# Kernel optimization log

Hardware: AMD Instinct MI355X
Metric: run time of the kernel (lower is better)

## Reference

```python
import jax, jax.numpy as jnp
import numpy as np

K = 3          # per-row / per-col topk, from init kwarg k
THRESHOLD = 0.0


def setup_inputs() -> dict:
    key = jax.random.key(0)
    k1, k2 = jax.random.split(key)
    P, R, S = 512, 256, 256
    matching_score_map = jax.random.normal(k1, (P, R, S), dtype=jnp.float32)
    node_corr_scores = jax.random.uniform(k2, (P,), dtype=jnp.float32)
    ref_knn_masks = jnp.ones((P, R), dtype=bool)
    src_knn_masks = jnp.ones((P, S), dtype=bool)
    return {
        "matching_score_map": matching_score_map,
        "node_corr_scores": node_corr_scores,
        "ref_knn_masks": ref_knn_masks,
        "src_knn_masks": src_knn_masks,
    }


def reference(matching_score_map, node_corr_scores, ref_knn_masks, src_knn_masks):
    # score map: exp of log-matching scores  [P, R, S]
    score = jnp.exp(matching_score_map)
    P, R, S = score.shape
    # valid correspondence mask  [P, R, S]
    corr_mask = ref_knn_masks[:, :, None] & src_knn_masks[:, None, :]

    p_idx = jnp.arange(P)[:, None, None]

    # topk along src axis (dim=2), scatter back into a zero map
    ref_vals, ref_idx = jax.lax.top_k(score, K)                      # [P, R, K]
    ref_score_map = jnp.zeros_like(score).at[
        p_idx, jnp.arange(R)[None, :, None], ref_idx
    ].set(ref_vals)

    # topk along ref axis (dim=1): transpose so it is the last axis
    src_vals, src_idx = jax.lax.top_k(score.transpose(0, 2, 1), K)   # [P, S, K]
    src_score_map = jnp.zeros_like(score).at[
        p_idx, src_idx, jnp.arange(S)[None, :, None]
    ].set(src_vals)

    ref_corr_map = (ref_score_map > THRESHOLD) & corr_mask
    src_corr_map = (src_score_map > THRESHOLD) & corr_mask

    score_map = (ref_score_map + src_score_map) * 0.5
    # mutual=False -> logical_or; conditional=False -> no node_corr_scores scaling
    corr_map = ref_corr_map | src_corr_map
    return score_map, corr_map
```

## Files before the change

### kernel.cpp

```cpp
#include <hip/hip_runtime.h>
#include <math.h>
#include <stdint.h>

#define Pn 512
#define Rn 256
#define Sn 256

typedef unsigned long long u64;
typedef unsigned int u32;

__device__ __forceinline__ u32 mono(float f) {
  u32 u = __float_as_uint(f);
  return (u & 0x80000000u) ? ~u : (u | 0x80000000u);
}
__device__ __forceinline__ float unmono(u32 m) {
  u32 bits = (m & 0x80000000u) ? (m & 0x7FFFFFFFu) : ~m;
  return __uint_as_float(bits);
}
__device__ __forceinline__ u64 makekey(float v, int idx) {
  return ((u64)mono(v) << 32) | (u32)(~(u32)idx);
}
__device__ __forceinline__ int key_idx(u64 k) { return (int)(~(u32)k); }
__device__ __forceinline__ float key_val(u64 k) { return unmono((u32)(k >> 32)); }

__device__ __forceinline__ void cswap(u64& a, u64& b) {
  const bool c = a > b;
  const u64 hi = c ? a : b;
  const u64 lo = c ? b : a;
  a = hi; b = lo;
}

__global__ void rowtop3_kernel(const float* __restrict__ score,
                               float* __restrict__ refv, int* __restrict__ refi) {
  const int row  = (blockIdx.x * blockDim.x + threadIdx.x) >> 6;
  const int lane = threadIdx.x & 63;
  const float4 v = reinterpret_cast<const float4*>(score + (size_t)row * Sn)[lane];
  const int b = lane * 4;
  u64 a0 = makekey(v.x, b + 0);
  u64 a1 = makekey(v.y, b + 1);
  u64 a2 = makekey(v.z, b + 2);
  u64 a3 = makekey(v.w, b + 3);
  cswap(a0, a1); cswap(a2, a3); cswap(a0, a2); cswap(a1, a3); cswap(a1, a2);
  u64 t0 = a0, t1 = a1, t2 = a2;

  u64 res0 = 0, res1 = 0, res2 = 0;
  #pragma unroll
  for (int j = 0; j < 3; ++j) {
    u64 m = t0;
    #pragma unroll
    for (int off = 1; off < 64; off <<= 1) {
      const u64 o = __shfl_xor(m, off);
      m = (o > m) ? o : m;
    }
    const bool hit = (t0 == m);
    t0 = hit ? t1 : t0;
    t1 = hit ? t2 : t1;
    t2 = hit ? 0ull : t2;
    if (j == 0) res0 = m; else if (j == 1) res1 = m; else res2 = m;
  }
  if (lane == 0) {
    const size_t o = (size_t)row * 3;
    refv[o + 0] = expf(key_val(res0)); refi[o + 0] = key_idx(res0);
    refv[o + 1] = expf(key_val(res1)); refi[o + 1] = key_idx(res1);
    refv[o + 2] = expf(key_val(res2)); refi[o + 2] = key_idx(res2);
  }
}

__global__ void coltop3_kernel(const float* __restrict__ score,
                               float* __restrict__ srcv, int* __restrict__ srci) {
  const int p = blockIdx.x;
  const int s = threadIdx.x;
  const float* base = score + (size_t)p * Rn * Sn + s;
  u64 t0 = 0, t1 = 0, t2 = 0;
  #pragma unroll 8
  for (int r = 0; r < Rn; ++r) {
    u64 k = makekey(base[(size_t)r * Sn], r);
    cswap(t0, k); cswap(t1, k); cswap(t2, k);
  }
  const size_t PS = (size_t)Pn * Sn;
  const size_t o  = (size_t)p * Sn + s;
  srcv[0 * PS + o] = expf(key_val(t0)); srci[0 * PS + o] = key_idx(t0);
  srcv[1 * PS + o] = expf(key_val(t1)); srci[1 * PS + o] = key_idx(t1);
  srcv[2 * PS + o] = expf(key_val(t2)); srci[2 * PS + o] = key_idx(t2);
}

__device__ __forceinline__ void compute_elem(
    int s, int r, bool rmask, int sm,
    float rv0, float rv1, float rv2, int ri0, int ri1, int ri2,
    float a0, int b0, float a1, int b1, float a2, int b2,
    float& oscore, float& ocorr) {
  const float rv = (s == ri0) ? rv0 : (s == ri1) ? rv1 : (s == ri2) ? rv2 : 0.0f;
  const float sv = (r == b0) ? a0 : (r == b1) ? a1 : (r == b2) ? a2 : 0.0f;
  oscore = 0.5f * (rv + sv);
  const bool m = rmask && (sm != 0);
  ocorr = (((rv > 0.0f) || (sv > 0.0f)) && m) ? 1.0f : 0.0f;
}

__global__ void write_kernel(
    const float* __restrict__ refv, const int* __restrict__ refi,
    const float* __restrict__ srcv, const int* __restrict__ srci,
    const int* __restrict__ rmaskp, const int* __restrict__ smaskp,
    float* __restrict__ out) {
  const int row  = blockIdx.x * 4 + (threadIdx.x >> 6);
  const int lane = threadIdx.x & 63;
  const int p = row >> 8;
  const int r = row & (Rn - 1);
  const size_t PS = (size_t)Pn * Sn;
  const size_t N  = (size_t)Pn * Rn * Sn;

  const size_t rb = (size_t)row * 3;
  const float rv0 = refv[rb + 0], rv1 = refv[rb + 1], rv2 = refv[rb + 2];
  const int   ri0 = refi[rb + 0], ri1 = refi[rb + 1], ri2 = refi[rb + 2];
  const bool  rmask = rmaskp[row] != 0;

  const float4 sv0 = reinterpret_cast<const float4*>(srcv + 0 * PS + (size_t)p * Sn)[lane];
  const float4 sv1 = reinterpret_cast<const float4*>(srcv + 1 * PS + (size_t)p * Sn)[lane];
  const float4 sv2 = reinterpret_cast<const float4*>(srcv + 2 * PS + (size_t)p * Sn)[lane];
  const int4   si0 = reinterpret_cast<const int4*>(srci + 0 * PS + (size_t)p * Sn)[lane];
  const int4   si1 = reinterpret_cast<const int4*>(srci + 1 * PS + (size_t)p * Sn)[lane];
  const int4   si2 = reinterpret_cast<const int4*>(srci + 2 * PS + (size_t)p * Sn)[lane];
  const int4   sm  = reinterpret_cast<const int4*>(smaskp + (size_t)p * Sn)[lane];

  const int sbase = lane * 4;
  float4 osc, oco;
  compute_elem(sbase + 0, r, rmask, sm.x, rv0, rv1, rv2, ri0, ri1, ri2,
               sv0.x, si0.x, sv1.x, si1.x, sv2.x, si2.x, osc.x, oco.x);
  compute_elem(sbase + 1, r, rmask, sm.y, rv0, rv1, rv2, ri0, ri1, ri2,
               sv0.y, si0.y, sv1.y, si1.y, sv2.y, si2.y, osc.y, oco.y);
  compute_elem(sbase + 2, r, rmask, sm.z, rv0, rv1, rv2, ri0, ri1, ri2,
               sv0.z, si0.z, sv1.z, si1.z, sv2.z, si2.z, osc.z, oco.z);
  compute_elem(sbase + 3, r, rmask, sm.w, rv0, rv1, rv2, ri0, ri1, ri2,
               sv0.w, si0.w, sv1.w, si1.w, sv2.w, si2.w, osc.w, oco.w);

  reinterpret_cast<float4*>(out + (size_t)row * Sn)[lane]     = osc;
  reinterpret_cast<float4*>(out + N + (size_t)row * Sn)[lane] = oco;
}

extern "C" void kernel_launch(void* const* d_in, const int* in_sizes, int n_in,
                              void* d_out, int out_size, void* d_ws, size_t ws_size,
                              hipStream_t stream) {
  const float* score = (const float*)d_in[0];
  const int* rmask = (const int*)d_in[2];
  const int* smask = (const int*)d_in[3];
  float* out = (float*)d_out;

  const size_t PR = (size_t)Pn * Rn;
  const size_t PS = (size_t)Pn * Sn;
  float* refv = (float*)d_ws;
  int*   refi = (int*)(refv + 3 * PR);
  float* srcv = (float*)(refi + 3 * PR);
  int*   srci = (int*)(srcv + 3 * PS);

  rowtop3_kernel<<<(Pn * Rn) / 4, 256, 0, stream>>>(score, refv, refi);
  coltop3_kernel<<<Pn, 256, 0, stream>>>(score, srcv, srci);
  write_kernel<<<(Pn * Rn) / 4, 256, 0, stream>>>(refv, refi, srcv, srci,
                                                  rmask, smask, out);
}
```

Baseline: 430.9 us.

## Fuse row top-3, column top-3 and output write into one per-batch kernel

Replaces three kernels with a single kernel that gives each batch slice to one 512-thread block. The block computes row and column top-3 results, keeps them in shared memory, and writes both output maps, so the global workspace round trip and two extra launches go away. The column scan is split across two thread halves and merged through shared memory to double its parallelism. The trade-off is that only 512 blocks cover the grid, and each block's output phase waits behind serial top-k work. The second read of the 256 KB tile for the column pass may also not stay in cache.

```diff
diff --git a/kernel.cpp b/kernel.cpp
--- a/kernel.cpp
+++ b/kernel.cpp
@@ -30,60 +30,6 @@
   a = hi; b = lo;
 }
 
-__global__ void rowtop3_kernel(const float* __restrict__ score,
-                               float* __restrict__ refv, int* __restrict__ refi) {
-  const int row  = (blockIdx.x * blockDim.x + threadIdx.x) >> 6;
-  const int lane = threadIdx.x & 63;
-  const float4 v = reinterpret_cast<const float4*>(score + (size_t)row * Sn)[lane];
-  const int b = lane * 4;
-  u64 a0 = makekey(v.x, b + 0);
-  u64 a1 = makekey(v.y, b + 1);
-  u64 a2 = makekey(v.z, b + 2);
-  u64 a3 = makekey(v.w, b + 3);
-  cswap(a0, a1); cswap(a2, a3); cswap(a0, a2); cswap(a1, a3); cswap(a1, a2);
-  u64 t0 = a0, t1 = a1, t2 = a2;
-
-  u64 res0 = 0, res1 = 0, res2 = 0;
-  #pragma unroll
-  for (int j = 0; j < 3; ++j) {
-    u64 m = t0;
-    #pragma unroll
-    for (int off = 1; off < 64; off <<= 1) {
-      const u64 o = __shfl_xor(m, off);
-      m = (o > m) ? o : m;
-    }
-    const bool hit = (t0 == m);
-    t0 = hit ? t1 : t0;
-    t1 = hit ? t2 : t1;
-    t2 = hit ? 0ull : t2;
-    if (j == 0) res0 = m; else if (j == 1) res1 = m; else res2 = m;
-  }
-  if (lane == 0) {
-    const size_t o = (size_t)row * 3;
-    refv[o + 0] = expf(key_val(res0)); refi[o + 0] = key_idx(res0);
-    refv[o + 1] = expf(key_val(res1)); refi[o + 1] = key_idx(res1);
-    refv[o + 2] = expf(key_val(res2)); refi[o + 2] = key_idx(res2);
-  }
-}
-
-__global__ void coltop3_kernel(const float* __restrict__ score,
-                               float* __restrict__ srcv, int* __restrict__ srci) {
-  const int p = blockIdx.x;
-  const int s = threadIdx.x;
-  const float* base = score + (size_t)p * Rn * Sn + s;
-  u64 t0 = 0, t1 = 0, t2 = 0;
-  #pragma unroll 8
-  for (int r = 0; r < Rn; ++r) {
-    u64 k = makekey(base[(size_t)r * Sn], r);
-    cswap(t0, k); cswap(t1, k); cswap(t2, k);
-  }
-  const size_t PS = (size_t)Pn * Sn;
-  const size_t o  = (size_t)p * Sn + s;
-  srcv[0 * PS + o] = expf(key_val(t0)); srci[0 * PS + o] = key_idx(t0);
-  srcv[1 * PS + o] = expf(key_val(t1)); srci[1 * PS + o] = key_idx(t1);
-  srcv[2 * PS + o] = expf(key_val(t2)); srci[2 * PS + o] = key_idx(t2);
-}
-
 __device__ __forceinline__ void compute_elem(
     int s, int r, bool rmask, int sm,
     float rv0, float rv1, float rv2, int ri0, int ri1, int ri2,
@@ -96,44 +42,122 @@
   ocorr = (((rv > 0.0f) || (sv > 0.0f)) && m) ? 1.0f : 0.0f;
 }
 
-__global__ void write_kernel(
-    const float* __restrict__ refv, const int* __restrict__ refi,
-    const float* __restrict__ srcv, const int* __restrict__ srci,
+__global__ __launch_bounds__(512) void fused_kernel(
+    const float* __restrict__ score,
     const int* __restrict__ rmaskp, const int* __restrict__ smaskp,
     float* __restrict__ out) {
-  const int row  = blockIdx.x * 4 + (threadIdx.x >> 6);
-  const int lane = threadIdx.x & 63;
-  const int p = row >> 8;
-  const int r = row & (Rn - 1);
-  const size_t PS = (size_t)Pn * Sn;
-  const size_t N  = (size_t)Pn * Rn * Sn;
+  const int p    = blockIdx.x;
+  const int tid  = threadIdx.x;
+  const int wave = tid >> 6;
+  const int lane = tid & 63;
 
-  const size_t rb = (size_t)row * 3;
-  const float rv0 = refv[rb + 0], rv1 = refv[rb + 1], rv2 = refv[rb + 2];
-  const int   ri0 = refi[rb + 0], ri1 = refi[rb + 1], ri2 = refi[rb + 2];
-  const bool  rmask = rmaskp[row] != 0;
+  __shared__ float rowv[3][Rn];
+  __shared__ int   rowi[3][Rn];
+  __shared__ u64   colk[3][Sn];
+  __shared__ float colv[3][Sn];
+  __shared__ int   coli[3][Sn];
+  __shared__ int   rmlds[Rn];
 
-  const float4 sv0 = reinterpret_cast<const float4*>(srcv + 0 * PS + (size_t)p * Sn)[lane];
-  const float4 sv1 = reinterpret_cast<const float4*>(srcv + 1 * PS + (size_t)p * Sn)[lane];
-  const float4 sv2 = reinterpret_cast<const float4*>(srcv + 2 * PS + (size_t)p * Sn)[lane];
-  const int4   si0 = reinterpret_cast<const int4*>(srci + 0 * PS + (size_t)p * Sn)[lane];
-  const int4   si1 = reinterpret_cast<const int4*>(srci + 1 * PS + (size_t)p * Sn)[lane];
-  const int4   si2 = reinterpret_cast<const int4*>(srci + 2 * PS + (size_t)p * Sn)[lane];
-  const int4   sm  = reinterpret_cast<const int4*>(smaskp + (size_t)p * Sn)[lane];
+  const float* tile = score + (size_t)p * Rn * Sn;
+
+  if (tid < Rn) rmlds[tid] = rmaskp[p * Rn + tid];
+
+  for (int i = 0; i < 32; ++i) {
+    const int r = wave * 32 + i;
+    const float4 v = reinterpret_cast<const float4*>(tile + (size_t)r * Sn)[lane];
+    const int b = lane * 4;
+    u64 a0 = makekey(v.x, b + 0);
+    u64 a1 = makekey(v.y, b + 1);
+    u64 a2 = makekey(v.z, b + 2);
+    u64 a3 = makekey(v.w, b + 3);
+    cswap(a0, a1); cswap(a2, a3); cswap(a0, a2); cswap(a1, a3); cswap(a1, a2);
+    u64 t0 = a0, t1 = a1, t2 = a2;
+
+    u64 res0 = 0, res1 = 0, res2 = 0;
+    #pragma unroll
+    for (int j = 0; j < 3; ++j) {
+      u64 m = t0;
+      #pragma unroll
+      for (int off = 1; off < 64; off <<= 1) {
+        const u64 o = __shfl_xor(m, off);
+        m = (o > m) ? o : m;
+      }
+      const bool hit = (t0 == m);
+      t0 = hit ? t1 : t0;
+      t1 = hit ? t2 : t1;
+      t2 = hit ? 0ull : t2;
+      if (j == 0) res0 = m; else if (j == 1) res1 = m; else res2 = m;
+    }
+    if (lane == 0) {
+      rowv[0][r] = expf(key_val(res0)); rowi[0][r] = key_idx(res0);
+      rowv[1][r] = expf(key_val(res1)); rowi[1][r] = key_idx(res1);
+      rowv[2][r] = expf(key_val(res2)); rowi[2][r] = key_idx(res2);
+    }
+  }
+
+  {
+    const int s = tid & (Sn - 1);
+    const int h = tid >> 8;
+    const float* base = tile + (size_t)h * 128 * Sn + s;
+    u64 t0 = 0, t1 = 0, t2 = 0;
+    #pragma unroll 8
+    for (int r = 0; r < 128; ++r) {
+      u64 k = makekey(base[(size_t)r * Sn], h * 128 + r);
+      cswap(t0, k); cswap(t1, k); cswap(t2, k);
+    }
+    if (h == 1) {
+      colk[0][s] = t0; colk[1][s] = t1; colk[2][s] = t2;
+    }
+    __syncthreads();
+    if (h == 0) {
+      u64 k;
+      k = colk[0][s]; cswap(t0, k); cswap(t1, k); cswap(t2, k);
+      k = colk[1][s]; cswap(t0, k); cswap(t1, k); cswap(t2, k);
+      k = colk[2][s]; cswap(t0, k); cswap(t1, k); cswap(t2, k);
+      colv[0][s] = expf(key_val(t0)); coli[0][s] = key_idx(t0);
+      colv[1][s] = expf(key_val(t1)); coli[1][s] = key_idx(t1);
+      colv[2][s] = expf(key_val(t2)); coli[2][s] = key_idx(t2);
+    }
+    __syncthreads();
+  }
 
   const int sbase = lane * 4;
-  float4 osc, oco;
-  compute_elem(sbase + 0, r, rmask, sm.x, rv0, rv1, rv2, ri0, ri1, ri2,
-               sv0.x, si0.x, sv1.x, si1.x, sv2.x, si2.x, osc.x, oco.x);
-  compute_elem(sbase + 1, r, rmask, sm.y, rv0, rv1, rv2, ri0, ri1, ri2,
-               sv0.y, si0.y, sv1.y, si1.y, sv2.y, si2.y, osc.y, oco.y);
-  compute_elem(sbase + 2, r, rmask, sm.z, rv0, rv1, rv2, ri0, ri1, ri2,
-               sv0.z, si0.z, sv1.z, si1.z, sv2.z, si2.z, osc.z, oco.z);
-  compute_elem(sbase + 3, r, rmask, sm.w, rv0, rv1, rv2, ri0, ri1, ri2,
-               sv0.w, si0.w, sv1.w, si1.w, sv2.w, si2.w, osc.w, oco.w);
+  float cv0x = colv[0][sbase + 0], cv0y = colv[0][sbase + 1],
+        cv0z = colv[0][sbase + 2], cv0w = colv[0][sbase + 3];
+  float cv1x = colv[1][sbase + 0], cv1y = colv[1][sbase + 1],
+        cv1z = colv[1][sbase + 2], cv1w = colv[1][sbase + 3];
+  float cv2x = colv[2][sbase + 0], cv2y = colv[2][sbase + 1],
+        cv2z = colv[2][sbase + 2], cv2w = colv[2][sbase + 3];
+  int ci0x = coli[0][sbase + 0], ci0y = coli[0][sbase + 1],
+      ci0z = coli[0][sbase + 2], ci0w = coli[0][sbase + 3];
+  int ci1x = coli[1][sbase + 0], ci1y = coli[1][sbase + 1],
+      ci1z = coli[1][sbase + 2], ci1w = coli[1][sbase + 3];
+  int ci2x = coli[2][sbase + 0], ci2y = coli[2][sbase + 1],
+      ci2z = coli[2][sbase + 2], ci2w = coli[2][sbase + 3];
+  const int4 sm = reinterpret_cast<const int4*>(smaskp + (size_t)p * Sn)[lane];
+  const size_t N = (size_t)Pn * Rn * Sn;
+  float* outp = out + (size_t)p * Rn * Sn;
 
-  reinterpret_cast<float4*>(out + (size_t)row * Sn)[lane]     = osc;
-  reinterpret_cast<float4*>(out + N + (size_t)row * Sn)[lane] = oco;
+  #pragma unroll 4
+  for (int i = 0; i < 32; ++i) {
+    const int r = wave * 32 + i;
+    const float rv0 = rowv[0][r], rv1 = rowv[1][r], rv2 = rowv[2][r];
+    const int   ri0 = rowi[0][r], ri1 = rowi[1][r], ri2 = rowi[2][r];
+    const bool  rm  = rmlds[r] != 0;
+
+    float4 osc, oco;
+    compute_elem(sbase + 0, r, rm, sm.x, rv0, rv1, rv2, ri0, ri1, ri2,
+                 cv0x, ci0x, cv1x, ci1x, cv2x, ci2x, osc.x, oco.x);
+    compute_elem(sbase + 1, r, rm, sm.y, rv0, rv1, rv2, ri0, ri1, ri2,
+                 cv0y, ci0y, cv1y, ci1y, cv2y, ci2y, osc.y, oco.y);
+    compute_elem(sbase + 2, r, rm, sm.z, rv0, rv1, rv2, ri0, ri1, ri2,
+                 cv0z, ci0z, cv1z, ci1z, cv2z, ci2z, osc.z, oco.z);
+    compute_elem(sbase + 3, r, rm, sm.w, rv0, rv1, rv2, ri0, ri1, ri2,
+                 cv0w, ci0w, cv1w, ci1w, cv2w, ci2w, osc.w, oco.w);
+
+    reinterpret_cast<float4*>(outp + (size_t)r * Sn)[lane]     = osc;
+    reinterpret_cast<float4*>(outp + N + (size_t)r * Sn)[lane] = oco;
+  }
 }
 
 extern "C" void kernel_launch(void* const* d_in, const int* in_sizes, int n_in,
@@ -144,15 +168,5 @@
   const int* smask = (const int*)d_in[3];
   float* out = (float*)d_out;
 
-  const size_t PR = (size_t)Pn * Rn;
-  const size_t PS = (size_t)Pn * Sn;
-  float* refv = (float*)d_ws;
-  int*   refi = (int*)(refv + 3 * PR);
-  float* srcv = (float*)(refi + 3 * PR);
-  int*   srci = (int*)(srcv + 3 * PS);
-
-  rowtop3_kernel<<<(Pn * Rn) / 4, 256, 0, stream>>>(score, refv, refi);
-  coltop3_kernel<<<Pn, 256, 0, stream>>>(score, srcv, srci);
-  write_kernel<<<(Pn * Rn) / 4, 256, 0, stream>>>(refv, refi, srcv, srci,
-                                                  rmask, smask, out);
+  fused_kernel<<<Pn, 512, 0, stream>>>(score, rmask, smask, out);
 }
```

After: 483.0 us. 1.12x slower.
